# Kernel tuning notes

Hardware: AMD Instinct MI355X
Metric: run time of the kernel (lower is better)

## Reference

```python
import jax, jax.numpy as jnp
import numpy as np


def setup_inputs() -> dict:
    key = jax.random.key(0)
    k1, k2 = jax.random.split(key)
    z = jax.random.normal(k1, (16, 128, 32, 32), dtype=jnp.float32)
    codes = jax.random.normal(k2, (8, 512, 16), dtype=jnp.float32)  # [latent_dim, num_codes, channel_dim]
    return {"z": z, "codes": codes}


def reference(z, codes):
    L, K, D = codes.shape          # latent_dim, num_codes, channel_dim
    B, C, H, W = z.shape           # C == L * D
    # permute to channels-last and split channels into (L, D)
    h = jnp.transpose(z, (0, 2, 3, 1)).reshape(B, H, W, L, D)
    # pairwise L2 distances via ||h||^2 - 2 h.W + ||W||^2 (avoids materializing [B,H,W,L,K,D])
    h2 = jnp.sum(h * h, axis=-1)                      # [B,H,W,L]
    w2 = jnp.sum(codes * codes, axis=-1)              # [L,K]
    cross = jnp.einsum('bhwld,lkd->bhwlk', h, codes)  # [B,H,W,L,K]
    d2 = h2[..., None] - 2.0 * cross + w2[None, None, None]
    distances = jnp.sqrt(jnp.maximum(d2, 1e-12))      # [B,H,W,L,K]
    # softmin over codes == softmax of negated distances
    probs = jax.nn.softmax(-distances, axis=4)
    soft_symbols = jnp.einsum('bhwlk,lkd->bhwld', probs, codes).reshape(B, H, W, C)
    # hard assignment: nearest code per latent dim
    idxes = jnp.argmin(distances, axis=4)             # [B,H,W,L]
    hard_symbols = codes[jnp.arange(L), idxes]        # [B,H,W,L,D]
    hard_symbols = hard_symbols.reshape(B, H, W, C)
    return (soft_symbols, hard_symbols, idxes)
```

## Files before the change

### kernel.cpp

```cpp
#include <hip/hip_runtime.h>
#include <hip/hip_bf16.h>

typedef float  f32x4  __attribute__((ext_vector_type(4)));
typedef short  s16x8  __attribute__((ext_vector_type(8)));
typedef __bf16 bf16x8 __attribute__((ext_vector_type(8)));

namespace {
constexpr int BHW = 16384, L = 8, K = 512, D = 16, HW = 1024, CH = 128;
constexpr int TPB = 512;
constexpr int PPB = 256;
constexpr size_t WS_CA_ELEMS = (size_t)L * K * 32;

__device__ __forceinline__ f32x4 mfma16(s16x8 a, s16x8 b, f32x4 c) {
  return __builtin_amdgcn_mfma_f32_16x16x32_bf16(
      __builtin_bit_cast(bf16x8, a), __builtin_bit_cast(bf16x8, b), c, 0, 0, 0);
}
__device__ __forceinline__ unsigned short bfh(float x) {
  return __builtin_bit_cast(unsigned short, __float2bfloat16(x));
}
__device__ __forceinline__ float bf2f(unsigned short u) {
  return __bfloat162float(__builtin_bit_cast(__hip_bfloat16, u));
}

__global__ void repack(const float* __restrict__ codes,
                       unsigned short* __restrict__ cA, float* __restrict__ w2g) {
  int i = blockIdx.x * 256 + threadIdx.x;
  const float* c = codes + (size_t)i * D;
  float s = 0.f;
  #pragma unroll
  for (int d = 0; d < D; ++d) s = fmaf(c[d], c[d], s);
  w2g[i] = s;
  int l = i >> 9, k = i & (K - 1);
  int ck = k >> 5, kloc = k & 31, g = kloc >> 3, w = kloc & 7, t = w >> 2, r = w & 3;
  int prow = ck * 32 + t * 16 + g * 4 + r;
  unsigned short* dst = cA + ((size_t)l * K + prow) * 32;
  #pragma unroll
  for (int d = 0; d < D; ++d) {
    unsigned short hi = bfh(c[d]);
    dst[d] = hi; dst[16 + d] = bfh(c[d] - bf2f(hi));
  }
}

__global__ __launch_bounds__(TPB, 4) void enc_mfma(
    const float* __restrict__ z,
    const float* __restrict__ codes,
    const unsigned short* __restrict__ cA,
    const float* __restrict__ w2g,
    float* __restrict__ out)
{
  __shared__ short cB[2][8192];
  __shared__ float w2s[K];
  __shared__ float h2s[PPB];
  __shared__ float ssum[8][32];
  __shared__ int   bks[8][32];

  const int tid  = threadIdx.x;
  const int l    = blockIdx.y;
  const int bx   = blockIdx.x;
  const int bimg = bx >> 2;
  const int yx0  = (bx & 3) * PPB;

  float* hstg = (float*)&cB[0][0];
  {
    const int i = tid & 255, dc = tid >> 8;
    #pragma unroll
    for (int it = 0; it < 8; ++it) {
      int d = dc * 8 + it;
      hstg[i * 17 + d] = z[((size_t)(bimg * CH + l * D + d)) * HW + yx0 + i];
    }
  }
  __syncthreads();

  const int wv   = __builtin_amdgcn_readfirstlane(tid >> 6);
  const int lane = tid & 63;
  const int cl   = lane & 15;
  const int g    = lane >> 4;
  const int pw   = wv * 32;

  if (tid < PPB) {
    float h2 = 0.f;
    #pragma unroll
    for (int d = 0; d < 16; ++d) { float v = hstg[tid * 17 + d]; h2 = fmaf(v, v, h2); }
    h2s[tid] = h2;
  }
  s16x8 B1a, B2a, B1b, B2b;
  {
    const int off = (g & 1) * 8;
    #pragma unroll
    for (int j = 0; j < 8; ++j) {
      float va = hstg[(pw + cl) * 17 + off + j];
      unsigned short ha = bfh(va);
      B1a[j] = (short)ha; B2a[j] = (short)bfh(va - bf2f(ha));
      float vb = hstg[(pw + 16 + cl) * 17 + off + j];
      unsigned short hb = bfh(vb);
      B1b[j] = (short)hb; B2b[j] = (short)bfh(vb - bf2f(hb));
    }
  }
  __syncthreads();
  const float h2a = h2s[pw + cl];
  const float h2b = h2s[pw + 16 + cl];

  {
    int k = tid, ck = k >> 5, kloc = k & 31, gg = kloc >> 3, w = kloc & 7, t = w >> 2, r = w & 3;
    int prow = ck * 32 + t * 16 + gg * 4 + r;
    const s16x8* src = (const s16x8*)(cA + ((size_t)l * K + prow) * 32);
    s16x8 h0 = src[0], h1 = src[1], l0 = src[2], l1 = src[3];
    int base = (ck * 4 + gg) * 128 + w;
    #pragma unroll
    for (int d = 0; d < 8; ++d) {
      cB[0][base + d * 8]       = h0[d];
      cB[1][base + d * 8]       = l0[d];
      cB[0][base + (d + 8) * 8] = h1[d];
      cB[1][base + (d + 8) * 8] = l1[d];
    }
    w2s[k] = w2g[l * K + k];
  }
  __syncthreads();

  const s16x8* Ab = (const s16x8*)(cA + (size_t)l * K * 32) + (cl * 4 + g);

  float m2A = 1e30f, mbA = 1e30f, sA = 0.f;
  float m2B = 1e30f, mbB = 1e30f, sB = 0.f;
  f32x4 pva0 = {0,0,0,0}, pva1 = {0,0,0,0}, pvb0 = {0,0,0,0}, pvb1 = {0,0,0,0};

  auto soft8 = [&](f32x4 T0, f32x4 T1, f32x4 W0, f32x4 W1, float h2, int ck,
                   float& m2, float& m2b, float& s) -> s16x8 {
    s16x8 PA;
    #pragma unroll
    for (int t = 0; t < 2; ++t) {
      #pragma unroll
      for (int r = 0; r < 4; ++r) {
        float T  = t ? T1[r] : T0[r];
        float Wk = t ? W1[r] : W0[r];
        float d2 = fmaf(-2.f, T, h2) + Wk;
        d2 = fmaxf(d2, 1e-12f);
        int kloc = ck * 32 + 8 * g + t * 4 + r;
        float key = __int_as_float((__float_as_int(d2) & 0xFFFFFE00) | kloc);
        m2b = __builtin_amdgcn_fmed3f(key, m2, m2b);
        m2  = fminf(m2, key);
        float dist = __builtin_amdgcn_sqrtf(d2);
        float w = __builtin_amdgcn_exp2f(dist * -1.44269504088896340736f);
        s += w;
        PA[t * 4 + r] = (short)bfh(w);
      }
    }
    return PA;
  };

  #pragma unroll 2
  for (int ck = 0; ck < 16; ++ck) {
    s16x8 A0 = Ab[ck * 128];
    s16x8 A1 = Ab[ck * 128 + 64];
    s16x8 Bh = *(const s16x8*)&cB[0][(ck * 4 + g) * 128 + cl * 8];
    s16x8 Bl = *(const s16x8*)&cB[1][(ck * 4 + g) * 128 + cl * 8];
    f32x4 W0 = *(const f32x4*)&w2s[ck * 32 + 8 * g];
    f32x4 W1 = *(const f32x4*)&w2s[ck * 32 + 8 * g + 4];

    f32x4 T0a = {0,0,0,0}, T1a = {0,0,0,0}, T0b = {0,0,0,0}, T1b = {0,0,0,0};
    T0a = mfma16(A0, B1a, T0a); T0a = mfma16(A0, B2a, T0a);
    T1a = mfma16(A1, B1a, T1a); T1a = mfma16(A1, B2a, T1a);
    T0b = mfma16(A0, B1b, T0b); T0b = mfma16(A0, B2b, T0b);
    T1b = mfma16(A1, B1b, T1b); T1b = mfma16(A1, B2b, T1b);

    s16x8 PAa = soft8(T0a, T1a, W0, W1, h2a, ck, m2A, mbA, sA);
    pva0 = mfma16(PAa, Bh, pva0);
    pva1 = mfma16(PAa, Bl, pva1);
    s16x8 PAb = soft8(T0b, T1b, W0, W1, h2b, ck, m2B, mbB, sB);
    pvb0 = mfma16(PAb, Bh, pvb0);
    pvb1 = mfma16(PAb, Bl, pvb1);
  }
  f32x4 pva = pva0 + pva1;
  f32x4 pvb = pvb0 + pvb1;

  #pragma unroll
  for (int off = 16; off < 64; off <<= 1) {
    sA += __shfl_xor(sA, off);
    float mo = __shfl_xor(m2A, off), mbo = __shfl_xor(mbA, off);
    mbA = fminf(fminf(mbA, mbo), fmaxf(m2A, mo));
    m2A = fminf(m2A, mo);
    sB += __shfl_xor(sB, off);
    float mo2 = __shfl_xor(m2B, off), mbo2 = __shfl_xor(mbB, off);
    mbB = fminf(fminf(mbB, mbo2), fmaxf(m2B, mo2));
    m2B = fminf(m2B, mo2);
  }
  int kaA = __float_as_int(m2A) & 511;
  int kaB = __float_as_int(m2B) & 511;
  bool trigA = (__int_as_float(__float_as_int(mbA) & 0xFFFFFE00) -
                __int_as_float(__float_as_int(m2A) & 0xFFFFFE00)) < 0.02f;
  bool trigB = (__int_as_float(__float_as_int(mbB) & 0xFFFFFE00) -
                __int_as_float(__float_as_int(m2B) & 0xFFFFFE00)) < 0.02f;

  if (lane < 16) {
    ssum[wv][lane] = sA;      bks[wv][lane] = kaA;
    ssum[wv][16 + lane] = sB; bks[wv][16 + lane] = kaB;
  }

  unsigned long long mask = __ballot(lane < 16 && trigA) |
                            (__ballot(lane < 16 && trigB) << 16);
  while (mask) {
    int pl = __ffsll((long long)mask) - 1; mask &= mask - 1;
    float hh[16];
    #pragma unroll
    for (int d = 0; d < 16; ++d)
      hh[d] = z[((size_t)(bimg * CH + l * D + d)) * HW + yx0 + pw + pl];
    float h2x = h2s[pw + pl];
    float bm = 1e30f; int bkk = 0;
    for (int rnd = 0; rnd < 8; ++rnd) {
      int k = rnd * 64 + lane;
      const float* cr = codes + ((size_t)l * K + k) * D;
      float cross = 0.f;
      #pragma unroll
      for (int d = 0; d < 16; ++d) cross = fmaf(hh[d], cr[d], cross);
      float d2 = (h2x - 2.f * cross) + w2g[l * K + k];
      d2 = fmaxf(d2, 1e-12f);
      float dist = sqrtf(d2);
      if (dist < bm) { bm = dist; bkk = k; }
    }
    #pragma unroll
    for (int off = 1; off < 64; off <<= 1) {
      float bo = __shfl_xor(bm, off); int ko = __shfl_xor(bkk, off);
      if (bo < bm || (bo == bm && ko < bkk)) { bm = bo; bkk = ko; }
    }
    if (lane == 0) bks[wv][pl] = bkk;
  }

  __syncthreads();
  const int pg0 = bimg * HW + yx0;
  f32x4 svA = *(const f32x4*)&ssum[wv][g * 4];
  f32x4 svB = *(const f32x4*)&ssum[wv][16 + g * 4];
  #pragma unroll
  for (int r = 0; r < 4; ++r) {
    out[(size_t)(pg0 + pw + g * 4 + r) * CH + l * D + cl]      = pva[r] * __builtin_amdgcn_rcpf(svA[r]);
    out[(size_t)(pg0 + pw + 16 + g * 4 + r) * CH + l * D + cl] = pvb[r] * __builtin_amdgcn_rcpf(svB[r]);
  }
  int kkA = bks[wv][cl];
  int kkB = bks[wv][16 + cl];
  float4 cvA = *(const float4*)&codes[((size_t)l * K + kkA) * D + g * 4];
  float4 cvB = *(const float4*)&codes[((size_t)l * K + kkB) * D + g * 4];
  *(float4*)&out[(size_t)BHW * CH + (size_t)(pg0 + pw + cl) * CH + l * D + g * 4]      = cvA;
  *(float4*)&out[(size_t)BHW * CH + (size_t)(pg0 + pw + 16 + cl) * CH + l * D + g * 4] = cvB;
  if (lane < 16) {
    out[(size_t)2 * BHW * CH + (size_t)(pg0 + pw + cl) * L + l]      = (float)kkA;
    out[(size_t)2 * BHW * CH + (size_t)(pg0 + pw + 16 + cl) * L + l] = (float)kkB;
  }
}
}

extern "C" void kernel_launch(void* const* d_in, const int* in_sizes, int n_in,
                              void* d_out, int out_size, void* d_ws, size_t ws_size,
                              hipStream_t stream) {
  const float* z     = (const float*)d_in[0];
  const float* codes = (const float*)d_in[1];
  float* out         = (float*)d_out;
  unsigned short* cA = (unsigned short*)d_ws;
  float* w2g         = (float*)((char*)d_ws + WS_CA_ELEMS * 2);

  repack<<<dim3(L * K / 256), 256, 0, stream>>>(codes, cA, w2g);
  dim3 grid(BHW / PPB, L);
  enc_mfma<<<grid, TPB, 0, stream>>>(z, codes, cA, w2g, out);
}
```

Before: 63.38 us.

## Split codebook across wave halves with LDS reduction, halve pixels per block

Each block now handles 128 pixels instead of 256. Its eight waves split into two halves, and each half processes half of the 512 codes for the same 32-pixel group. The second half writes its partial PV accumulators, softmax sums and min/second-min keys to LDS, where the first half merges them before the refine and output path. This doubles the grid to 1024 blocks and allows 8 blocks per CU, raising parallelism and shortening each wave's serial loop. In exchange it adds two barriers, LDS traffic, and repeated per-block codebook staging.

```diff
diff --git a/kernel.cpp b/kernel.cpp
--- a/kernel.cpp
+++ b/kernel.cpp
@@ -8,7 +8,7 @@
 namespace {
 constexpr int BHW = 16384, L = 8, K = 512, D = 16, HW = 1024, CH = 128;
 constexpr int TPB = 512;
-constexpr int PPB = 256;
+constexpr int PPB = 128;
 constexpr size_t WS_CA_ELEMS = (size_t)L * K * 32;
 
 __device__ __forceinline__ f32x4 mfma16(s16x8 a, s16x8 b, f32x4 c) {
@@ -41,7 +41,7 @@
   }
 }
 
-__global__ __launch_bounds__(TPB, 4) void enc_mfma(
+__global__ __launch_bounds__(TPB, 8) void enc_mfma(
     const float* __restrict__ z,
     const float* __restrict__ codes,
     const unsigned short* __restrict__ cA,
@@ -51,21 +51,21 @@
   __shared__ short cB[2][8192];
   __shared__ float w2s[K];
   __shared__ float h2s[PPB];
-  __shared__ float ssum[8][32];
-  __shared__ int   bks[8][32];
+  __shared__ float ssum[4][32];
+  __shared__ int   bks[4][32];
 
   const int tid  = threadIdx.x;
   const int l    = blockIdx.y;
   const int bx   = blockIdx.x;
-  const int bimg = bx >> 2;
-  const int yx0  = (bx & 3) * PPB;
+  const int bimg = bx >> 3;
+  const int yx0  = (bx & 7) * PPB;
 
   float* hstg = (float*)&cB[0][0];
   {
-    const int i = tid & 255, dc = tid >> 8;
-    #pragma unroll
-    for (int it = 0; it < 8; ++it) {
-      int d = dc * 8 + it;
+    const int i = tid & 127, dc = tid >> 7;
+    #pragma unroll
+    for (int it = 0; it < 4; ++it) {
+      int d = dc * 4 + it;
       hstg[i * 17 + d] = z[((size_t)(bimg * CH + l * D + d)) * HW + yx0 + i];
     }
   }
@@ -75,7 +75,9 @@
   const int lane = tid & 63;
   const int cl   = lane & 15;
   const int g    = lane >> 4;
-  const int pw   = wv * 32;
+  const int pgp  = wv & 3;
+  const int half = wv >> 2;
+  const int pw   = pgp * 32;
 
   if (tid < PPB) {
     float h2 = 0.f;
@@ -147,8 +149,10 @@
     return PA;
   };
 
+  const int ck0 = half * 8;
   #pragma unroll 2
-  for (int ck = 0; ck < 16; ++ck) {
+  for (int cki = 0; cki < 8; ++cki) {
+    const int ck = ck0 + cki;
     s16x8 A0 = Ab[ck * 128];
     s16x8 A1 = Ab[ck * 128 + 64];
     s16x8 Bh = *(const s16x8*)&cB[0][(ck * 4 + g) * 128 + cl * 8];
@@ -183,65 +187,100 @@
     mbB = fminf(fminf(mbB, mbo2), fmaxf(m2B, mo2));
     m2B = fminf(m2B, mo2);
   }
-  int kaA = __float_as_int(m2A) & 511;
-  int kaB = __float_as_int(m2B) & 511;
-  bool trigA = (__int_as_float(__float_as_int(mbA) & 0xFFFFFE00) -
-                __int_as_float(__float_as_int(m2A) & 0xFFFFFE00)) < 0.02f;
-  bool trigB = (__int_as_float(__float_as_int(mbB) & 0xFFFFFE00) -
-                __int_as_float(__float_as_int(m2B) & 0xFFFFFE00)) < 0.02f;
-
-  if (lane < 16) {
-    ssum[wv][lane] = sA;      bks[wv][lane] = kaA;
-    ssum[wv][16 + lane] = sB; bks[wv][16 + lane] = kaB;
-  }
-
-  unsigned long long mask = __ballot(lane < 16 && trigA) |
-                            (__ballot(lane < 16 && trigB) << 16);
-  while (mask) {
-    int pl = __ffsll((long long)mask) - 1; mask &= mask - 1;
-    float hh[16];
-    #pragma unroll
-    for (int d = 0; d < 16; ++d)
-      hh[d] = z[((size_t)(bimg * CH + l * D + d)) * HW + yx0 + pw + pl];
-    float h2x = h2s[pw + pl];
-    float bm = 1e30f; int bkk = 0;
-    for (int rnd = 0; rnd < 8; ++rnd) {
-      int k = rnd * 64 + lane;
-      const float* cr = codes + ((size_t)l * K + k) * D;
-      float cross = 0.f;
+
+  float* pvbuf = (float*)&cB[0][0];
+  float* smbuf = pvbuf + 128 * 17;
+  __syncthreads();
+  if (half == 1) {
+    #pragma unroll
+    for (int r = 0; r < 4; ++r) {
+      pvbuf[(pw + g * 4 + r) * 17 + cl]      = pva[r];
+      pvbuf[(pw + 16 + g * 4 + r) * 17 + cl] = pvb[r];
+    }
+    if (lane < 16) {
+      float* d0 = &smbuf[(pw + cl) * 3];
+      d0[0] = sA; d0[1] = m2A; d0[2] = mbA;
+      float* d1 = &smbuf[(pw + 16 + cl) * 3];
+      d1[0] = sB; d1[1] = m2B; d1[2] = mbB;
+    }
+  }
+  __syncthreads();
+  if (half == 0) {
+    #pragma unroll
+    for (int r = 0; r < 4; ++r) {
+      pva[r] += pvbuf[(pw + g * 4 + r) * 17 + cl];
+      pvb[r] += pvbuf[(pw + 16 + g * 4 + r) * 17 + cl];
+    }
+    if (lane < 16) {
+      const float* s0 = &smbuf[(pw + cl) * 3];
+      sA += s0[0];
+      mbA = fminf(fminf(mbA, s0[2]), fmaxf(m2A, s0[1]));
+      m2A = fminf(m2A, s0[1]);
+      const float* s1 = &smbuf[(pw + 16 + cl) * 3];
+      sB += s1[0];
+      mbB = fminf(fminf(mbB, s1[2]), fmaxf(m2B, s1[1]));
+      m2B = fminf(m2B, s1[1]);
+    }
+
+    int kaA = __float_as_int(m2A) & 511;
+    int kaB = __float_as_int(m2B) & 511;
+    bool trigA = (__int_as_float(__float_as_int(mbA) & 0xFFFFFE00) -
+                  __int_as_float(__float_as_int(m2A) & 0xFFFFFE00)) < 0.02f;
+    bool trigB = (__int_as_float(__float_as_int(mbB) & 0xFFFFFE00) -
+                  __int_as_float(__float_as_int(m2B) & 0xFFFFFE00)) < 0.02f;
+
+    if (lane < 16) {
+      ssum[pgp][lane] = sA;      bks[pgp][lane] = kaA;
+      ssum[pgp][16 + lane] = sB; bks[pgp][16 + lane] = kaB;
+    }
+
+    unsigned long long mask = __ballot(lane < 16 && trigA) |
+                              (__ballot(lane < 16 && trigB) << 16);
+    while (mask) {
+      int pl = __ffsll((long long)mask) - 1; mask &= mask - 1;
+      float hh[16];
       #pragma unroll
-      for (int d = 0; d < 16; ++d) cross = fmaf(hh[d], cr[d], cross);
-      float d2 = (h2x - 2.f * cross) + w2g[l * K + k];
-      d2 = fmaxf(d2, 1e-12f);
-      float dist = sqrtf(d2);
-      if (dist < bm) { bm = dist; bkk = k; }
-    }
-    #pragma unroll
-    for (int off = 1; off < 64; off <<= 1) {
-      float bo = __shfl_xor(bm, off); int ko = __shfl_xor(bkk, off);
-      if (bo < bm || (bo == bm && ko < bkk)) { bm = bo; bkk = ko; }
-    }
-    if (lane == 0) bks[wv][pl] = bkk;
-  }
-
-  __syncthreads();
-  const int pg0 = bimg * HW + yx0;
-  f32x4 svA = *(const f32x4*)&ssum[wv][g * 4];
-  f32x4 svB = *(const f32x4*)&ssum[wv][16 + g * 4];
-  #pragma unroll
-  for (int r = 0; r < 4; ++r) {
-    out[(size_t)(pg0 + pw + g * 4 + r) * CH + l * D + cl]      = pva[r] * __builtin_amdgcn_rcpf(svA[r]);
-    out[(size_t)(pg0 + pw + 16 + g * 4 + r) * CH + l * D + cl] = pvb[r] * __builtin_amdgcn_rcpf(svB[r]);
-  }
-  int kkA = bks[wv][cl];
-  int kkB = bks[wv][16 + cl];
-  float4 cvA = *(const float4*)&codes[((size_t)l * K + kkA) * D + g * 4];
-  float4 cvB = *(const float4*)&codes[((size_t)l * K + kkB) * D + g * 4];
-  *(float4*)&out[(size_t)BHW * CH + (size_t)(pg0 + pw + cl) * CH + l * D + g * 4]      = cvA;
-  *(float4*)&out[(size_t)BHW * CH + (size_t)(pg0 + pw + 16 + cl) * CH + l * D + g * 4] = cvB;
-  if (lane < 16) {
-    out[(size_t)2 * BHW * CH + (size_t)(pg0 + pw + cl) * L + l]      = (float)kkA;
-    out[(size_t)2 * BHW * CH + (size_t)(pg0 + pw + 16 + cl) * L + l] = (float)kkB;
+      for (int d = 0; d < 16; ++d)
+        hh[d] = z[((size_t)(bimg * CH + l * D + d)) * HW + yx0 + pw + pl];
+      float h2x = h2s[pw + pl];
+      float bm = 1e30f; int bkk = 0;
+      for (int rnd = 0; rnd < 8; ++rnd) {
+        int k = rnd * 64 + lane;
+        const float* cr = codes + ((size_t)l * K + k) * D;
+        float cross = 0.f;
+        #pragma unroll
+        for (int d = 0; d < 16; ++d) cross = fmaf(hh[d], cr[d], cross);
+        float d2 = (h2x - 2.f * cross) + w2g[l * K + k];
+        d2 = fmaxf(d2, 1e-12f);
+        float dist = sqrtf(d2);
+        if (dist < bm) { bm = dist; bkk = k; }
+      }
+      #pragma unroll
+      for (int off = 1; off < 64; off <<= 1) {
+        float bo = __shfl_xor(bm, off); int ko = __shfl_xor(bkk, off);
+        if (bo < bm || (bo == bm && ko < bkk)) { bm = bo; bkk = ko; }
+      }
+      if (lane == 0) bks[pgp][pl] = bkk;
+    }
+
+    const int pg0 = bimg * HW + yx0;
+    f32x4 svA = *(const f32x4*)&ssum[pgp][g * 4];
+    f32x4 svB = *(const f32x4*)&ssum[pgp][16 + g * 4];
+    #pragma unroll
+    for (int r = 0; r < 4; ++r) {
+      out[(size_t)(pg0 + pw + g * 4 + r) * CH + l * D + cl]      = pva[r] * __builtin_amdgcn_rcpf(svA[r]);
+      out[(size_t)(pg0 + pw + 16 + g * 4 + r) * CH + l * D + cl] = pvb[r] * __builtin_amdgcn_rcpf(svB[r]);
+    }
+    int kkA = bks[pgp][cl];
+    int kkB = bks[pgp][16 + cl];
+    float4 cvA = *(const float4*)&codes[((size_t)l * K + kkA) * D + g * 4];
+    float4 cvB = *(const float4*)&codes[((size_t)l * K + kkB) * D + g * 4];
+    *(float4*)&out[(size_t)BHW * CH + (size_t)(pg0 + pw + cl) * CH + l * D + g * 4]      = cvA;
+    *(float4*)&out[(size_t)BHW * CH + (size_t)(pg0 + pw + 16 + cl) * CH + l * D + g * 4] = cvB;
+    if (lane < 16) {
+      out[(size_t)2 * BHW * CH + (size_t)(pg0 + pw + cl) * L + l]      = (float)kkA;
+      out[(size_t)2 * BHW * CH + (size_t)(pg0 + pw + 16 + cl) * L + l] = (float)kkB;
+    }
   }
 }
 }
```

Measured after the change: 169.6 us. 2.68x slower.

## Pipeline distance MFMAs one tile ahead and compute softmax sum via MFMA

Applied to the files above, without the earlier changes.

The main loop is software-pipelined: the cross-product MFMAs for the next code tile are issued, at raised wave priority, before the softmin arithmetic of the current tile, so matrix and vector work can overlap. Codebook and activation norms are pre-scaled by log2(e)^2, so the square root directly gives the base-2 exponent argument and one multiply per element goes away. The softmax denominator is now accumulated by an extra MFMA against a ones vector instead of per-lane adds and shuffles. The near-tie threshold is raised to match the scaled distances; the costs are more registers for the prefetched tiles and a bf16-rounded denominator.

```diff
diff --git a/kernel.cpp b/kernel.cpp
--- a/kernel.cpp
+++ b/kernel.cpp
@@ -9,7 +9,10 @@
 constexpr int BHW = 16384, L = 8, K = 512, D = 16, HW = 1024, CH = 128;
 constexpr int TPB = 512;
 constexpr int PPB = 256;
-constexpr size_t WS_CA_ELEMS = (size_t)L * K * 32;
+constexpr float KAPPA = 2.0813689810056077f;
+constexpr size_t WS_CA_BYTES = (size_t)L * K * 32 * 2;
+constexpr size_t WS_W2_BYTES = (size_t)L * K * 4;
+constexpr size_t WS_W2K_OFF  = WS_CA_BYTES + WS_W2_BYTES;
 
 __device__ __forceinline__ f32x4 mfma16(s16x8 a, s16x8 b, f32x4 c) {
   return __builtin_amdgcn_mfma_f32_16x16x32_bf16(
@@ -23,13 +26,15 @@
 }
 
 __global__ void repack(const float* __restrict__ codes,
-                       unsigned short* __restrict__ cA, float* __restrict__ w2g) {
+                       unsigned short* __restrict__ cA,
+                       float* __restrict__ w2g, float* __restrict__ w2k) {
   int i = blockIdx.x * 256 + threadIdx.x;
   const float* c = codes + (size_t)i * D;
   float s = 0.f;
   #pragma unroll
   for (int d = 0; d < D; ++d) s = fmaf(c[d], c[d], s);
   w2g[i] = s;
+  w2k[i] = KAPPA * s;
   int l = i >> 9, k = i & (K - 1);
   int ck = k >> 5, kloc = k & 31, g = kloc >> 3, w = kloc & 7, t = w >> 2, r = w & 3;
   int prow = ck * 32 + t * 16 + g * 4 + r;
@@ -46,6 +51,7 @@
     const float* __restrict__ codes,
     const unsigned short* __restrict__ cA,
     const float* __restrict__ w2g,
+    const float* __restrict__ w2k,
     float* __restrict__ out)
 {
   __shared__ short cB[2][8192];
@@ -97,8 +103,8 @@
     }
   }
   __syncthreads();
-  const float h2a = h2s[pw + cl];
-  const float h2b = h2s[pw + 16 + cl];
+  const float h2ka = KAPPA * h2s[pw + cl];
+  const float h2kb = KAPPA * h2s[pw + 16 + cl];
 
   {
     int k = tid, ck = k >> 5, kloc = k & 31, gg = kloc >> 3, w = kloc & 7, t = w >> 2, r = w & 3;
@@ -113,18 +119,21 @@
       cB[0][base + (d + 8) * 8] = h1[d];
       cB[1][base + (d + 8) * 8] = l1[d];
     }
-    w2s[k] = w2g[l * K + k];
+    w2s[k] = w2k[l * K + k];
   }
   __syncthreads();
 
   const s16x8* Ab = (const s16x8*)(cA + (size_t)l * K * 32) + (cl * 4 + g);
-
-  float m2A = 1e30f, mbA = 1e30f, sA = 0.f;
-  float m2B = 1e30f, mbB = 1e30f, sB = 0.f;
-  f32x4 pva0 = {0,0,0,0}, pva1 = {0,0,0,0}, pvb0 = {0,0,0,0}, pvb1 = {0,0,0,0};
-
-  auto soft8 = [&](f32x4 T0, f32x4 T1, f32x4 W0, f32x4 W1, float h2, int ck,
-                   float& m2, float& m2b, float& s) -> s16x8 {
+  const s16x8 ONES = {(short)0x3F80, (short)0x3F80, (short)0x3F80, (short)0x3F80,
+                      (short)0x3F80, (short)0x3F80, (short)0x3F80, (short)0x3F80};
+
+  float m2A = 1e30f, mbA = 1e30f;
+  float m2B = 1e30f, mbB = 1e30f;
+  f32x4 pva0 = {0,0,0,0}, pva1 = {0,0,0,0}, pvsA = {0,0,0,0};
+  f32x4 pvb0 = {0,0,0,0}, pvb1 = {0,0,0,0}, pvsB = {0,0,0,0};
+
+  auto soft8 = [&](const f32x4& T0, const f32x4& T1, const f32x4& W0, const f32x4& W1,
+                   float h2k, int ct, float& m2, float& m2b) -> s16x8 {
     s16x8 PA;
     #pragma unroll
     for (int t = 0; t < 2; ++t) {
@@ -132,53 +141,64 @@
       for (int r = 0; r < 4; ++r) {
         float T  = t ? T1[r] : T0[r];
         float Wk = t ? W1[r] : W0[r];
-        float d2 = fmaf(-2.f, T, h2) + Wk;
+        float d2 = fmaf(-2.f * KAPPA, T, h2k) + Wk;
         d2 = fmaxf(d2, 1e-12f);
-        int kloc = ck * 32 + 8 * g + t * 4 + r;
+        int kloc = ct * 32 + 8 * g + t * 4 + r;
         float key = __int_as_float((__float_as_int(d2) & 0xFFFFFE00) | kloc);
         m2b = __builtin_amdgcn_fmed3f(key, m2, m2b);
         m2  = fminf(m2, key);
         float dist = __builtin_amdgcn_sqrtf(d2);
-        float w = __builtin_amdgcn_exp2f(dist * -1.44269504088896340736f);
-        s += w;
+        float w = __builtin_amdgcn_exp2f(-dist);
         PA[t * 4 + r] = (short)bfh(w);
       }
     }
     return PA;
   };
 
+  f32x4 T0a_p = {0,0,0,0}, T1a_p = {0,0,0,0}, T0b_p = {0,0,0,0}, T1b_p = {0,0,0,0};
+  {
+    s16x8 A0 = Ab[0], A1 = Ab[64];
+    __builtin_amdgcn_s_setprio(1);
+    T0a_p = mfma16(A0, B1a, T0a_p); T0a_p = mfma16(A0, B2a, T0a_p);
+    T1a_p = mfma16(A1, B1a, T1a_p); T1a_p = mfma16(A1, B2a, T1a_p);
+    T0b_p = mfma16(A0, B1b, T0b_p); T0b_p = mfma16(A0, B2b, T0b_p);
+    T1b_p = mfma16(A1, B1b, T1b_p); T1b_p = mfma16(A1, B2b, T1b_p);
+    __builtin_amdgcn_s_setprio(0);
+  }
+
   #pragma unroll 2
-  for (int ck = 0; ck < 16; ++ck) {
-    s16x8 A0 = Ab[ck * 128];
-    s16x8 A1 = Ab[ck * 128 + 64];
-    s16x8 Bh = *(const s16x8*)&cB[0][(ck * 4 + g) * 128 + cl * 8];
-    s16x8 Bl = *(const s16x8*)&cB[1][(ck * 4 + g) * 128 + cl * 8];
-    f32x4 W0 = *(const f32x4*)&w2s[ck * 32 + 8 * g];
-    f32x4 W1 = *(const f32x4*)&w2s[ck * 32 + 8 * g + 4];
-
-    f32x4 T0a = {0,0,0,0}, T1a = {0,0,0,0}, T0b = {0,0,0,0}, T1b = {0,0,0,0};
-    T0a = mfma16(A0, B1a, T0a); T0a = mfma16(A0, B2a, T0a);
-    T1a = mfma16(A1, B1a, T1a); T1a = mfma16(A1, B2a, T1a);
-    T0b = mfma16(A0, B1b, T0b); T0b = mfma16(A0, B2b, T0b);
-    T1b = mfma16(A1, B1b, T1b); T1b = mfma16(A1, B2b, T1b);
-
-    s16x8 PAa = soft8(T0a, T1a, W0, W1, h2a, ck, m2A, mbA, sA);
-    pva0 = mfma16(PAa, Bh, pva0);
-    pva1 = mfma16(PAa, Bl, pva1);
-    s16x8 PAb = soft8(T0b, T1b, W0, W1, h2b, ck, m2B, mbB, sB);
-    pvb0 = mfma16(PAb, Bh, pvb0);
-    pvb1 = mfma16(PAb, Bl, pvb1);
+  for (int ct = 0; ct < 16; ++ct) {
+    f32x4 T0a_c = {0,0,0,0}, T1a_c = {0,0,0,0}, T0b_c = {0,0,0,0}, T1b_c = {0,0,0,0};
+    if (ct < 15) {
+      s16x8 A0 = Ab[(ct + 1) * 128], A1 = Ab[(ct + 1) * 128 + 64];
+      __builtin_amdgcn_s_setprio(1);
+      T0a_c = mfma16(A0, B1a, T0a_c); T0a_c = mfma16(A0, B2a, T0a_c);
+      T1a_c = mfma16(A1, B1a, T1a_c); T1a_c = mfma16(A1, B2a, T1a_c);
+      T0b_c = mfma16(A0, B1b, T0b_c); T0b_c = mfma16(A0, B2b, T0b_c);
+      T1b_c = mfma16(A1, B1b, T1b_c); T1b_c = mfma16(A1, B2b, T1b_c);
+      __builtin_amdgcn_s_setprio(0);
+    }
+    s16x8 Bh = *(const s16x8*)&cB[0][(ct * 4 + g) * 128 + cl * 8];
+    s16x8 Bl = *(const s16x8*)&cB[1][(ct * 4 + g) * 128 + cl * 8];
+    f32x4 W0 = *(const f32x4*)&w2s[ct * 32 + 8 * g];
+    f32x4 W1 = *(const f32x4*)&w2s[ct * 32 + 8 * g + 4];
+
+    s16x8 PAa = soft8(T0a_p, T1a_p, W0, W1, h2ka, ct, m2A, mbA);
+    s16x8 PAb = soft8(T0b_p, T1b_p, W0, W1, h2kb, ct, m2B, mbB);
+    __builtin_amdgcn_s_setprio(1);
+    pva0 = mfma16(PAa, Bh, pva0); pva1 = mfma16(PAa, Bl, pva1); pvsA = mfma16(PAa, ONES, pvsA);
+    pvb0 = mfma16(PAb, Bh, pvb0); pvb1 = mfma16(PAb, Bl, pvb1); pvsB = mfma16(PAb, ONES, pvsB);
+    __builtin_amdgcn_s_setprio(0);
+    T0a_p = T0a_c; T1a_p = T1a_c; T0b_p = T0b_c; T1b_p = T1b_c;
   }
   f32x4 pva = pva0 + pva1;
   f32x4 pvb = pvb0 + pvb1;
 
   #pragma unroll
   for (int off = 16; off < 64; off <<= 1) {
-    sA += __shfl_xor(sA, off);
     float mo = __shfl_xor(m2A, off), mbo = __shfl_xor(mbA, off);
     mbA = fminf(fminf(mbA, mbo), fmaxf(m2A, mo));
     m2A = fminf(m2A, mo);
-    sB += __shfl_xor(sB, off);
     float mo2 = __shfl_xor(m2B, off), mbo2 = __shfl_xor(mbB, off);
     mbB = fminf(fminf(mbB, mbo2), fmaxf(m2B, mo2));
     m2B = fminf(m2B, mo2);
@@ -186,14 +206,18 @@
   int kaA = __float_as_int(m2A) & 511;
   int kaB = __float_as_int(m2B) & 511;
   bool trigA = (__int_as_float(__float_as_int(mbA) & 0xFFFFFE00) -
-                __int_as_float(__float_as_int(m2A) & 0xFFFFFE00)) < 0.02f;
+                __int_as_float(__float_as_int(m2A) & 0xFFFFFE00)) < 0.045f;
   bool trigB = (__int_as_float(__float_as_int(mbB) & 0xFFFFFE00) -
-                __int_as_float(__float_as_int(m2B) & 0xFFFFFE00)) < 0.02f;
-
-  if (lane < 16) {
-    ssum[wv][lane] = sA;      bks[wv][lane] = kaA;
-    ssum[wv][16 + lane] = sB; bks[wv][16 + lane] = kaB;
-  }
+                __int_as_float(__float_as_int(m2B) & 0xFFFFFE00)) < 0.045f;
+
+  if (cl == 0) {
+    #pragma unroll
+    for (int r = 0; r < 4; ++r) {
+      ssum[wv][g * 4 + r]      = pvsA[r];
+      ssum[wv][16 + g * 4 + r] = pvsB[r];
+    }
+  }
+  if (lane < 16) { bks[wv][lane] = kaA; bks[wv][16 + lane] = kaB; }
 
   unsigned long long mask = __ballot(lane < 16 && trigA) |
                             (__ballot(lane < 16 && trigB) << 16);
@@ -253,9 +277,10 @@
   const float* codes = (const float*)d_in[1];
   float* out         = (float*)d_out;
   unsigned short* cA = (unsigned short*)d_ws;
-  float* w2g         = (float*)((char*)d_ws + WS_CA_ELEMS * 2);
-
-  repack<<<dim3(L * K / 256), 256, 0, stream>>>(codes, cA, w2g);
+  float* w2g         = (float*)((char*)d_ws + WS_CA_BYTES);
+  float* w2k         = (float*)((char*)d_ws + WS_W2K_OFF);
+
+  repack<<<dim3(L * K / 256), 256, 0, stream>>>(codes, cA, w2g, w2k);
   dim3 grid(BHW / PPB, L);
-  enc_mfma<<<grid, TPB, 0, stream>>>(z, codes, cA, w2g, out);
-}
+  enc_mfma<<<grid, TPB, 0, stream>>>(z, codes, cA, w2g, w2k, out);
+}
```

Result: no change. 63.75 us (+0.6%).
